# Kernel tuning notes

Hardware: AMD Instinct MI355X
Metric: run time of the kernel (lower is better)

## Reference

```python
import math
import jax, jax.numpy as jnp
import numpy as np

B, T, D = 2, 2048, 2048
DH, NQ, NKV = 128, 16, 4
QPG = NQ // NKV  # queries per group = 4
ROPE_BASE = 10000.0
YARN_SCALE = 2.0
ORIG_MAX_LEN = 4096
BETA_FAST, BETA_SLOW = 32.0, 1.0
EPS = 1.1920929e-07  # torch.finfo(float32).eps, RMSNorm default
MSCALE = 0.1 * math.log(YARN_SCALE) + 1.0
ATTN_SCALE = 1.0 / (MSCALE * math.sqrt(DH))


def _yarn_inv_freq():
    inv_freq = 1.0 / ROPE_BASE ** (np.arange(0, DH, 2, dtype=np.float32) / DH)
    wavelengths = 2.0 * math.pi / inv_freq
    low_w = ORIG_MAX_LEN / BETA_SLOW
    high_w = ORIG_MAX_LEN / BETA_FAST
    gamma = np.clip((low_w - wavelengths) / (low_w - high_w), 0.0, 1.0)
    return (gamma * inv_freq + (1.0 - gamma) * inv_freq / YARN_SCALE).astype(np.float32)


def setup_inputs() -> dict:
    key = jax.random.key(0)
    k0, k1, k2, k3 = jax.random.split(key, 4)
    x = jax.random.normal(k0, (B, T, D), jnp.float32)
    Wq = jax.random.normal(k1, (D, DH * NQ), jnp.float32) * 0.02
    Wkv = jax.random.normal(k2, (D, 2 * DH * NKV), jnp.float32) * 0.02
    Wout = jax.random.normal(k3, (DH * NQ, D), jnp.float32) * 0.02
    q_norm_w = jnp.ones((DH,), jnp.float32)
    k_norm_w = jnp.ones((DH,), jnp.float32)
    inv_freq = jnp.asarray(_yarn_inv_freq())
    return {"x": x, "Wq": Wq, "Wkv": Wkv, "Wout": Wout,
            "q_norm_w": q_norm_w, "k_norm_w": k_norm_w, "inv_freq": inv_freq}


def _rmsnorm(x, w):
    ms = jnp.mean(jnp.square(x), axis=-1, keepdims=True)
    return x * jax.lax.rsqrt(ms + EPS) * w


def _apply_rope(x, inv_freq):
    # x: (..., T, DH)
    t = jnp.arange(x.shape[-2], dtype=inv_freq.dtype)
    freqs = jnp.outer(t, inv_freq)               # (T, DH//2)
    emb = jnp.concatenate([freqs, freqs], -1)     # (T, DH)
    cos, sin = jnp.cos(emb), jnp.sin(emb)
    half = x.shape[-1] // 2
    x_rot = jnp.concatenate([-x[..., half:], x[..., :half]], -1)
    return x * cos + x_rot * sin


def reference(x, Wq, Wkv, Wout, q_norm_w, k_norm_w, inv_freq):
    q = x @ Wq                                    # (B, T, NQ*DH)
    kv = x @ Wkv                                  # (B, T, 2*NKV*DH)
    k, v = jnp.split(kv, 2, axis=-1)              # each (B, T, NKV*DH)
    # b t (qpg g d) -> b qpg g t d
    q = q.reshape(B, T, QPG, NKV, DH).transpose(0, 2, 3, 1, 4)
    # b t (g d) -> b g t d
    k = k.reshape(B, T, NKV, DH).transpose(0, 2, 1, 3)
    v = v.reshape(B, T, NKV, DH).transpose(0, 2, 1, 3)
    q = _apply_rope(_rmsnorm(q, q_norm_w), inv_freq)
    k = _apply_rope(_rmsnorm(k, k_norm_w), inv_freq)
    scores = jnp.einsum('bqgtd,bgsd->bqgts', q, k) * ATTN_SCALE
    causal = jnp.tril(jnp.ones((T, T), bool))
    scores = jnp.where(causal, scores, -jnp.inf)
    attn = jax.nn.softmax(scores, axis=-1)
    out = jnp.einsum('bqgts,bgsd->bqgtd', attn, v)
    # b qpg g t d -> b t (qpg g d)
    out = out.transpose(0, 3, 1, 2, 4).reshape(B, T, NQ * DH)
    return out @ Wout
```

## Files before the change

### kernel.cpp

```cpp
#include <hip/hip_runtime.h>
#include <math.h>


typedef __attribute__((ext_vector_type(8))) short s16x8;
typedef __attribute__((ext_vector_type(4))) float f32x4;
typedef __attribute__((ext_vector_type(4))) unsigned int u32x4;

__device__ __forceinline__ unsigned short f2bf(float x) {
  union { float f; unsigned int u; } v; v.f = x;
  return (unsigned short)((v.u + 0x7FFFu + ((v.u >> 16) & 1u)) >> 16);
}

__device__ __forceinline__ float bf2f(unsigned short x) {
  union { unsigned int u; float f; } v; v.u = (unsigned int)x << 16;
  return v.f;
}

__device__ __forceinline__ unsigned int cvt_pk_bf16(float lo, float hi) {
  unsigned int r;
  asm("v_cvt_pk_bf16_f32 %0, %1, %2" : "=v"(r) : "v"(lo), "v"(hi));
  return r;
}

#define GLD_LDS16(g, l)                                            \
  __builtin_amdgcn_global_load_lds(                                \
      (const __attribute__((address_space(1))) void*)(g),          \
      (__attribute__((address_space(3))) void*)(l), 16, 0, 0)

__device__ __forceinline__ void wtrans_body(const float* __restrict__ in,
                                            unsigned short* __restrict__ out,
                                            int R, int C, int bx, int by,
                                            unsigned short lt[64][65]) {
  const int r0 = bx * 64, c0 = by * 64;
  const int j = threadIdx.x & 63, i4 = threadIdx.x >> 6;
#pragma unroll
  for (int p = 0; p < 16; ++p) {
    int i = p * 4 + i4;
    lt[i][j] = f2bf(in[(size_t)(r0 + i) * C + c0 + j]);
  }
  __syncthreads();
#pragma unroll
  for (int p = 0; p < 16; ++p) {
    int i = p * 4 + i4;
    out[(size_t)(c0 + i) * R + r0 + j] = lt[j][i];
  }
}

__global__ __launch_bounds__(256) void prep1_k(const float* __restrict__ x,
                                               const float* __restrict__ Wq,
                                               const float* __restrict__ Wkv,
                                               const float* __restrict__ Wout,
                                               const float* __restrict__ invf,
                                               unsigned short* __restrict__ xb,
                                               unsigned short* __restrict__ wqkvt,
                                               unsigned short* __restrict__ wot,
                                               float2* __restrict__ cstab) {
  __shared__ unsigned short lt[64][65];
  const int bid = blockIdx.x;
  if (bid < 8192) {
    int i = bid * 256 + threadIdx.x;
    float4 v = ((const float4*)x)[i];
    unsigned long long pack = (unsigned long long)f2bf(v.x)
                            | ((unsigned long long)f2bf(v.y) << 16)
                            | ((unsigned long long)f2bf(v.z) << 32)
                            | ((unsigned long long)f2bf(v.w) << 48);
    ((unsigned long long*)xb)[i] = pack;
  } else if (bid < 9216) {
    int b2 = bid - 8192;
    wtrans_body(Wq, wqkvt, 2048, 2048, b2 & 31, b2 >> 5, lt);
  } else if (bid < 9728) {
    int b2 = bid - 9216;
    wtrans_body(Wkv, wqkvt + (size_t)2048 * 2048, 2048, 1024, b2 & 31, b2 >> 5, lt);
  } else if (bid < 10752) {
    int b2 = bid - 9728;
    wtrans_body(Wout, wot, 2048, 2048, b2 & 31, b2 >> 5, lt);
  } else {
    int i = (bid - 10752) * 256 + threadIdx.x;
    int t = i >> 6, f = i & 63;
    float s, c;
    sincosf((float)t * invf[f], &s, &c);
    cstab[i] = make_float2(c, s);
  }
}

template <int OUTBF>
__global__ __launch_bounds__(256) void gemm_bt_t(const unsigned short* __restrict__ A,
                                                 const unsigned short* __restrict__ Bt,
                                                 void* __restrict__ Cv,
                                                 int M, int N, int K) {
  __shared__ alignas(16) unsigned short sA[2][128][32];
  __shared__ alignas(16) unsigned short sB[2][128][32];
  const int tid = threadIdx.x;
  const int lane = tid & 63;
  const int w = tid >> 6;
  const int wm = (w >> 1) * 64, wn = (w & 1) * 64;
  const int nwg = gridDim.x * gridDim.y;
  int bid = blockIdx.y * gridDim.x + blockIdx.x;
  bid = (bid & 7) * (nwg >> 3) + (bid >> 3);
  const int m0 = (bid % gridDim.x) * 128, n0 = (bid / gridDim.x) * 128;
  const int l15 = lane & 15, lhi = lane >> 4;
  f32x4 acc[4][4];
#pragma unroll
  for (int i = 0; i < 4; ++i)
#pragma unroll
    for (int j = 0; j < 4; ++j) acc[i][j] = (f32x4){0.f, 0.f, 0.f, 0.f};
  const int row = tid >> 2;
  const int srcslot = (tid & 3) ^ ((row >> 1) & 3);
  const unsigned short* gA0 = A + (size_t)(m0 + row) * K + srcslot * 8;
  const unsigned short* gA1 = A + (size_t)(m0 + 64 + row) * K + srcslot * 8;
  const unsigned short* gB0 = Bt + (size_t)(n0 + row) * K + srcslot * 8;
  const unsigned short* gB1 = Bt + (size_t)(n0 + 64 + row) * K + srcslot * 8;
  char* ldsA = (char*)&sA[0][0][0] + w * 1024;
  char* ldsB = (char*)&sB[0][0][0] + w * 1024;
  auto STAGE = [&](int bb, int k0) {
    GLD_LDS16(gA0 + k0, ldsA + bb * 8192);
    GLD_LDS16(gA1 + k0, ldsA + bb * 8192 + 4096);
    GLD_LDS16(gB0 + k0, ldsB + bb * 8192);
    GLD_LDS16(gB1 + k0, ldsB + bb * 8192 + 4096);
  };
  const int sphys = (lhi ^ ((l15 >> 1) & 3)) * 8;
  const int nt = K >> 5;
  STAGE(0, 0);
  __syncthreads();
  int cur = 0;
  for (int t = 0; t < nt; ++t) {
    if (t + 1 < nt) STAGE(cur ^ 1, (t + 1) * 32);
    s16x8 af[4], bfr[4];
#pragma unroll
    for (int i = 0; i < 4; ++i) af[i] = *(const s16x8*)&sA[cur][wm + i * 16 + l15][sphys];
#pragma unroll
    for (int j = 0; j < 4; ++j) bfr[j] = *(const s16x8*)&sB[cur][wn + j * 16 + l15][sphys];
#pragma unroll
    for (int i = 0; i < 4; ++i)
#pragma unroll
      for (int j = 0; j < 4; ++j)
        acc[i][j] = __builtin_amdgcn_mfma_f32_16x16x32_bf16(af[i], bfr[j], acc[i][j], 0, 0, 0);
    __syncthreads();
    cur ^= 1;
  }
  const int col0 = n0 + wn + l15;
  const int row00 = m0 + wm + lhi * 4;
  if (OUTBF) {
    unsigned short* C = (unsigned short*)Cv;
#pragma unroll
    for (int i = 0; i < 4; ++i)
#pragma unroll
      for (int j = 0; j < 4; ++j)
#pragma unroll
        for (int r = 0; r < 4; ++r)
          C[(size_t)(row00 + i * 16 + r) * N + col0 + j * 16] = f2bf(acc[i][j][r]);
  } else {
    float* C = (float*)Cv;
#pragma unroll
    for (int i = 0; i < 4; ++i)
#pragma unroll
      for (int j = 0; j < 4; ++j)
#pragma unroll
        for (int r = 0; r < 4; ++r)
          C[(size_t)(row00 + i * 16 + r) * N + col0 + j * 16] = acc[i][j][r];
  }
}

__global__ __launch_bounds__(256) void prep2_k(const unsigned short* __restrict__ qkvb,
                                               const float* __restrict__ qw,
                                               const float* __restrict__ kw,
                                               const float2* __restrict__ cstab,
                                               unsigned short* __restrict__ qT,
                                               unsigned short* __restrict__ kT,
                                               unsigned short* __restrict__ vT) {
  __shared__ unsigned short lt[64][65];
  const int bid = blockIdx.x;
  if (bid < 20480) {
    constexpr float FOLD =
        (float)(1.4426950408889634 / ((0.1 * 0.6931471805599453 + 1.0) * 11.313708498984761));
    int wid = bid * 4 + (threadIdx.x >> 6);
    int lane = threadIdx.x & 63;
    const unsigned short* src; const float* wgt; unsigned short* dst;
    int t; float fold;
    if (wid < 65536) {
      int bt = wid >> 4, h = wid & 15;
      int b = bt >> 11; t = bt & 2047;
      src = qkvb + (size_t)bt * 3072 + h * 128;
      wgt = qw;
      dst = qT + ((size_t)(b * 16 + h) * 2048 + t) * 128;
      fold = FOLD;
    } else {
      int id = wid - 65536;
      int bt = id >> 2, g = id & 3;
      int b = bt >> 11; t = bt & 2047;
      src = qkvb + (size_t)bt * 3072 + 2048 + g * 128;
      wgt = kw;
      dst = kT + ((size_t)(b * 4 + g) * 2048 + t) * 128;
      fold = 1.0f;
    }
    unsigned int vv = ((const unsigned int*)src)[lane];
    float vx = bf2f((unsigned short)(vv & 0xffff));
    float vy = bf2f((unsigned short)(vv >> 16));
    float ss = vx * vx + vy * vy;
#pragma unroll
    for (int m = 32; m; m >>= 1) ss += __shfl_xor(ss, m);
    float rs = rsqrtf(ss * (1.0f / 128.0f) + 1.1920929e-07f);
    float2 wv = ((const float2*)wgt)[lane];
    float xn0 = vx * rs * wv.x;
    float xn1 = vy * rs * wv.y;
    float px = __shfl_xor(xn0, 32);
    float py = __shfl_xor(xn1, 32);
    float sgn = (lane < 32) ? -1.0f : 1.0f;
    int f0 = (2 * lane) & 63;
    float4 cs = ((const float4*)cstab)[((size_t)t * 64 + f0) >> 1];
    float r0 = (xn0 * cs.x + sgn * px * cs.y) * fold;
    float r1 = (xn1 * cs.z + sgn * py * cs.w) * fold;
    unsigned int packed = (unsigned int)f2bf(r0) | ((unsigned int)f2bf(r1) << 16);
    ((unsigned int*)dst)[lane] = packed;
  } else {
    int b2 = bid - 20480;
    const int tt0 = (b2 & 31) * 64;
    const int dd0 = ((b2 >> 5) & 1) * 64;
    const int z = b2 >> 6;
    const int b = z >> 2, g = z & 3;
    const int j = threadIdx.x & 63, i4 = threadIdx.x >> 6;
    const unsigned short* src = qkvb + (size_t)b * 2048 * 3072 + 2560 + g * 128 + dd0;
#pragma unroll
    for (int p = 0; p < 16; ++p) {
      int i = p * 4 + i4;
      lt[i][j] = src[(size_t)(tt0 + i) * 3072 + j];
    }
    __syncthreads();
    unsigned short* dst = vT + ((size_t)(b * 4 + g) * 128 + dd0) * 2048 + tt0;
    const int jp = (j & 32) | (((j & 15) >> 2) << 3) | (((j >> 4) & 1) << 2) | (j & 3);
#pragma unroll
    for (int p = 0; p < 16; ++p) {
      int d = p * 4 + i4;
      dst[(size_t)d * 2048 + jp] = lt[j][d];
    }
  }
}

__global__ __launch_bounds__(256) void attn_k(const unsigned short* __restrict__ qT,
                                              const unsigned short* __restrict__ kT,
                                              const unsigned short* __restrict__ vT,
                                              unsigned short* __restrict__ ao) {
  __shared__ alignas(16) unsigned short sK2[2][64][128];
  __shared__ alignas(16) unsigned short sV2[2][128][64];
  const int tid = threadIdx.x;
  const int lane = tid & 63;
  const int w = tid >> 6;
  const int l15 = lane & 15, lhi = lane >> 4;
  const int l8 = lane >> 3;
  const int bid = blockIdx.x;
  const int xg = bid & 7;
  const int b = xg >> 2, g = xg & 3;
  const int hh = (bid >> 3) & 3;
  const int h = hh * 4 + g;
  const int qt = 31 - (bid >> 5);
  const int q0 = qt * 64;
  const unsigned short* Qb = qT + ((size_t)(b * 16 + h) * 2048) * 128;
  const unsigned short* Kb = kT + ((size_t)(b * 4 + g) * 2048) * 128;
  const unsigned short* Vb = vT + ((size_t)(b * 4 + g) * 128) * 2048;

  s16x8 qfr[4];
#pragma unroll
  for (int ks = 0; ks < 4; ++ks)
    qfr[ks] = *(const s16x8*)(Qb + (size_t)(q0 + w * 16 + l15) * 128 + ks * 32 + lhi * 8);

  const int sgK = l15 ^ ((w * 4 + lhi) & 7);
  const int sgV = (lane & 7) ^ (l8 & 7);
  char* ldsK = (char*)&sK2[0][0][0] + w * 1024;
  char* ldsV = (char*)&sV2[0][0][0] + w * 1024;
  auto STAGEKV = [&](int bb, int kt) {
#pragma unroll
    for (int p = 0; p < 4; ++p) {
      GLD_LDS16(Kb + (size_t)(kt * 64 + p * 16 + w * 4 + lhi) * 128 + sgK * 8,
                ldsK + bb * 16384 + p * 4096);
      GLD_LDS16(Vb + (size_t)(p * 32 + w * 8 + l8) * 2048 + kt * 64 + sgV * 8,
                ldsV + bb * 16384 + p * 4096);
    }
  };
  const int xr = l15 & 7;

  f32x4 o[8];
#pragma unroll
  for (int i = 0; i < 8; ++i) o[i] = (f32x4){0.f, 0.f, 0.f, 0.f};
  f32x4 o9 = (f32x4){0.f, 0.f, 0.f, 0.f};
  s16x8 ones;
#pragma unroll
  for (int j = 0; j < 8; ++j) ones[j] = (short)0x3F80;

  STAGEKV(0, 0);
  int cur = 0;
  for (int kt = 0; kt <= qt; ++kt) {
    asm volatile("s_waitcnt vmcnt(0)" ::: "memory");
    __syncthreads();
    if (kt < qt) STAGEKV(cur ^ 1, kt + 1);
    f32x4 s[4];
#pragma unroll
    for (int jn = 0; jn < 4; ++jn) s[jn] = (f32x4){-16.f, -16.f, -16.f, -16.f};
#pragma unroll
    for (int ks = 0; ks < 4; ++ks)
#pragma unroll
      for (int jn = 0; jn < 4; ++jn) {
        s16x8 ak = *(const s16x8*)&sK2[cur][jn * 16 + l15][((ks * 4 + lhi) ^ xr) * 8];
        s[jn] = __builtin_amdgcn_mfma_f32_16x16x32_bf16(ak, qfr[ks], s[jn], 0, 0, 0);
      }
    if (kt == qt) {
#pragma unroll
      for (int jn = 0; jn < 4; ++jn)
#pragma unroll
        for (int r = 0; r < 4; ++r)
          if (jn * 16 + lhi * 4 + r > w * 16 + l15) s[jn][r] = -INFINITY;
    }
    float pp[4][4];
#pragma unroll
    for (int jn = 0; jn < 4; ++jn)
#pragma unroll
      for (int r = 0; r < 4; ++r) pp[jn][r] = exp2f(s[jn][r]);
    union { s16x8 v; unsigned int d[4]; } pa0, pa1;
#pragma unroll
    for (int d = 0; d < 2; ++d) {
      pa0.d[d]     = cvt_pk_bf16(pp[0][2 * d], pp[0][2 * d + 1]);
      pa0.d[2 + d] = cvt_pk_bf16(pp[1][2 * d], pp[1][2 * d + 1]);
      pa1.d[d]     = cvt_pk_bf16(pp[2][2 * d], pp[2][2 * d + 1]);
      pa1.d[2 + d] = cvt_pk_bf16(pp[3][2 * d], pp[3][2 * d + 1]);
    }
    o9 = __builtin_amdgcn_mfma_f32_16x16x32_bf16(pa0.v, ones, o9, 0, 0, 0);
    o9 = __builtin_amdgcn_mfma_f32_16x16x32_bf16(pa1.v, ones, o9, 0, 0, 0);
#pragma unroll
    for (int nt = 0; nt < 8; ++nt) {
      s16x8 vb0 = *(const s16x8*)&sV2[cur][nt * 16 + l15][(lhi ^ xr) * 8];
      o[nt] = __builtin_amdgcn_mfma_f32_16x16x32_bf16(pa0.v, vb0, o[nt], 0, 0, 0);
    }
#pragma unroll
    for (int nt = 0; nt < 8; ++nt) {
      s16x8 vb1 = *(const s16x8*)&sV2[cur][nt * 16 + l15][((lhi + 4) ^ xr) * 8];
      o[nt] = __builtin_amdgcn_mfma_f32_16x16x32_bf16(pa1.v, vb1, o[nt], 0, 0, 0);
    }
    cur ^= 1;
  }
#pragma unroll
  for (int r = 0; r < 4; ++r) {
    float invr = 1.0f / o9[r];
    int t = q0 + w * 16 + lhi * 4 + r;
    size_t base = ((size_t)b * 2048 + t) * 2048 + h * 128;
#pragma unroll
    for (int nt = 0; nt < 8; ++nt)
      ao[base + nt * 16 + l15] = f2bf(o[nt][r] * invr);
  }
}

extern "C" void kernel_launch(void* const* d_in, const int* in_sizes, int n_in,
                              void* d_out, int out_size, void* d_ws, size_t ws_size,
                              hipStream_t stream) {
  (void)in_sizes; (void)n_in; (void)out_size; (void)ws_size;
  const float* x    = (const float*)d_in[0];
  const float* Wq   = (const float*)d_in[1];
  const float* Wkv  = (const float*)d_in[2];
  const float* Wout = (const float*)d_in[3];
  const float* qw   = (const float*)d_in[4];
  const float* kw   = (const float*)d_in[5];
  const float* invf = (const float*)d_in[6];
  float* out = (float*)d_out;

  char* ws = (char*)d_ws;
  size_t off = 0;
  auto alloc = [&](size_t bytes) -> void* {
    void* p = ws + off; off += (bytes + 255) & ~(size_t)255; return p;
  };
  unsigned short* xb    = (unsigned short*)alloc((size_t)4096 * 2048 * 2);
  unsigned short* wqkvt = (unsigned short*)alloc((size_t)3072 * 2048 * 2);
  unsigned short* wot   = (unsigned short*)alloc((size_t)2048 * 2048 * 2);
  unsigned short* qkvb  = (unsigned short*)alloc((size_t)4096 * 3072 * 2);
  float2* cstab = (float2*)alloc((size_t)2048 * 64 * 8);
  unsigned short* qT = (unsigned short*)alloc((size_t)2 * 16 * 2048 * 128 * 2);
  unsigned short* kT = (unsigned short*)alloc((size_t)2 * 4 * 2048 * 128 * 2);
  unsigned short* vT = (unsigned short*)alloc((size_t)2 * 4 * 128 * 2048 * 2);
  unsigned short* ao = (unsigned short*)alloc((size_t)4096 * 2048 * 2);

  prep1_k<<<11264, 256, 0, stream>>>(x, Wq, Wkv, Wout, invf, xb, wqkvt, wot, cstab);
  gemm_bt_t<1><<<dim3(32, 24), 256, 0, stream>>>(xb, wqkvt, qkvb, 4096, 3072, 2048);
  prep2_k<<<20992, 256, 0, stream>>>(qkvb, qw, kw, cstab, qT, kT, vT);
  attn_k<<<1024, 256, 0, stream>>>(qT, kT, vT, ao);
  gemm_bt_t<0><<<dim3(32, 16), 256, 0, stream>>>(ao, wot, out, 4096, 2048, 2048);
}
```

Before: 193.6 us.

## Double attention query tile to 128 rows per block to reuse K/V tiles

```diff
diff --git a/kernel.cpp b/kernel.cpp
--- a/kernel.cpp
+++ b/kernel.cpp
@@ -252,16 +252,20 @@
   const int b = xg >> 2, g = xg & 3;
   const int hh = (bid >> 3) & 3;
   const int h = hh * 4 + g;
-  const int qt = 31 - (bid >> 5);
-  const int q0 = qt * 64;
+  const int u = bid >> 5;
+  const int qt = (u < 8) ? (15 - u) : (u - 8);
+  const int q0 = qt * 128;
   const unsigned short* Qb = qT + ((size_t)(b * 16 + h) * 2048) * 128;
   const unsigned short* Kb = kT + ((size_t)(b * 4 + g) * 2048) * 128;
   const unsigned short* Vb = vT + ((size_t)(b * 4 + g) * 128) * 2048;
 
-  s16x8 qfr[4];
-#pragma unroll
-  for (int ks = 0; ks < 4; ++ks)
-    qfr[ks] = *(const s16x8*)(Qb + (size_t)(q0 + w * 16 + l15) * 128 + ks * 32 + lhi * 8);
+  s16x8 qfr[2][4];
+#pragma unroll
+  for (int jq = 0; jq < 2; ++jq)
+#pragma unroll
+    for (int ks = 0; ks < 4; ++ks)
+      qfr[jq][ks] = *(const s16x8*)(Qb +
+          (size_t)(q0 + w * 32 + jq * 16 + l15) * 128 + ks * 32 + lhi * 8);
 
   const int sgK = l15 ^ ((w * 4 + lhi) & 7);
   const int sgV = (lane & 7) ^ (l8 & 7);
@@ -278,73 +282,89 @@
   };
   const int xr = l15 & 7;
 
-  f32x4 o[8];
-#pragma unroll
-  for (int i = 0; i < 8; ++i) o[i] = (f32x4){0.f, 0.f, 0.f, 0.f};
-  f32x4 o9 = (f32x4){0.f, 0.f, 0.f, 0.f};
+  f32x4 o[2][8];
+#pragma unroll
+  for (int jq = 0; jq < 2; ++jq)
+#pragma unroll
+    for (int i = 0; i < 8; ++i) o[jq][i] = (f32x4){0.f, 0.f, 0.f, 0.f};
+  f32x4 o9[2] = {(f32x4){0.f, 0.f, 0.f, 0.f}, (f32x4){0.f, 0.f, 0.f, 0.f}};
   s16x8 ones;
 #pragma unroll
   for (int j = 0; j < 8; ++j) ones[j] = (short)0x3F80;
 
+  const int ktmax = 2 * qt + 1;
   STAGEKV(0, 0);
   int cur = 0;
-  for (int kt = 0; kt <= qt; ++kt) {
+  for (int kt = 0; kt <= ktmax; ++kt) {
     asm volatile("s_waitcnt vmcnt(0)" ::: "memory");
     __syncthreads();
-    if (kt < qt) STAGEKV(cur ^ 1, kt + 1);
-    f32x4 s[4];
-#pragma unroll
-    for (int jn = 0; jn < 4; ++jn) s[jn] = (f32x4){-16.f, -16.f, -16.f, -16.f};
+    if (kt < ktmax) STAGEKV(cur ^ 1, kt + 1);
+    f32x4 s[2][4];
+#pragma unroll
+    for (int jq = 0; jq < 2; ++jq)
+#pragma unroll
+      for (int jn = 0; jn < 4; ++jn) s[jq][jn] = (f32x4){-16.f, -16.f, -16.f, -16.f};
 #pragma unroll
     for (int ks = 0; ks < 4; ++ks)
 #pragma unroll
       for (int jn = 0; jn < 4; ++jn) {
         s16x8 ak = *(const s16x8*)&sK2[cur][jn * 16 + l15][((ks * 4 + lhi) ^ xr) * 8];
-        s[jn] = __builtin_amdgcn_mfma_f32_16x16x32_bf16(ak, qfr[ks], s[jn], 0, 0, 0);
+        s[0][jn] = __builtin_amdgcn_mfma_f32_16x16x32_bf16(ak, qfr[0][ks], s[0][jn], 0, 0, 0);
+        s[1][jn] = __builtin_amdgcn_mfma_f32_16x16x32_bf16(ak, qfr[1][ks], s[1][jn], 0, 0, 0);
       }
-    if (kt == qt) {
+    if (kt >= 2 * qt) {
+#pragma unroll
+      for (int jq = 0; jq < 2; ++jq)
+#pragma unroll
+        for (int jn = 0; jn < 4; ++jn)
+#pragma unroll
+          for (int r = 0; r < 4; ++r)
+            if (kt * 64 + jn * 16 + lhi * 4 + r > q0 + w * 32 + jq * 16 + l15)
+              s[jq][jn][r] = -INFINITY;
+    }
+    union { s16x8 v; unsigned int d[4]; } pa[2][2];
+#pragma unroll
+    for (int jq = 0; jq < 2; ++jq) {
+      float pp[4][4];
 #pragma unroll
       for (int jn = 0; jn < 4; ++jn)
 #pragma unroll
-        for (int r = 0; r < 4; ++r)
-          if (jn * 16 + lhi * 4 + r > w * 16 + l15) s[jn][r] = -INFINITY;
-    }
-    float pp[4][4];
-#pragma unroll
-    for (int jn = 0; jn < 4; ++jn)
-#pragma unroll
-      for (int r = 0; r < 4; ++r) pp[jn][r] = exp2f(s[jn][r]);
-    union { s16x8 v; unsigned int d[4]; } pa0, pa1;
-#pragma unroll
-    for (int d = 0; d < 2; ++d) {
-      pa0.d[d]     = cvt_pk_bf16(pp[0][2 * d], pp[0][2 * d + 1]);
-      pa0.d[2 + d] = cvt_pk_bf16(pp[1][2 * d], pp[1][2 * d + 1]);
-      pa1.d[d]     = cvt_pk_bf16(pp[2][2 * d], pp[2][2 * d + 1]);
-      pa1.d[2 + d] = cvt_pk_bf16(pp[3][2 * d], pp[3][2 * d + 1]);
-    }
-    o9 = __builtin_amdgcn_mfma_f32_16x16x32_bf16(pa0.v, ones, o9, 0, 0, 0);
-    o9 = __builtin_amdgcn_mfma_f32_16x16x32_bf16(pa1.v, ones, o9, 0, 0, 0);
+        for (int r = 0; r < 4; ++r) pp[jn][r] = exp2f(s[jq][jn][r]);
+#pragma unroll
+      for (int d = 0; d < 2; ++d) {
+        pa[jq][0].d[d]     = cvt_pk_bf16(pp[0][2 * d], pp[0][2 * d + 1]);
+        pa[jq][0].d[2 + d] = cvt_pk_bf16(pp[1][2 * d], pp[1][2 * d + 1]);
+        pa[jq][1].d[d]     = cvt_pk_bf16(pp[2][2 * d], pp[2][2 * d + 1]);
+        pa[jq][1].d[2 + d] = cvt_pk_bf16(pp[3][2 * d], pp[3][2 * d + 1]);
+      }
+      o9[jq] = __builtin_amdgcn_mfma_f32_16x16x32_bf16(pa[jq][0].v, ones, o9[jq], 0, 0, 0);
+      o9[jq] = __builtin_amdgcn_mfma_f32_16x16x32_bf16(pa[jq][1].v, ones, o9[jq], 0, 0, 0);
+    }
 #pragma unroll
     for (int nt = 0; nt < 8; ++nt) {
       s16x8 vb0 = *(const s16x8*)&sV2[cur][nt * 16 + l15][(lhi ^ xr) * 8];
-      o[nt] = __builtin_amdgcn_mfma_f32_16x16x32_bf16(pa0.v, vb0, o[nt], 0, 0, 0);
+      o[0][nt] = __builtin_amdgcn_mfma_f32_16x16x32_bf16(pa[0][0].v, vb0, o[0][nt], 0, 0, 0);
+      o[1][nt] = __builtin_amdgcn_mfma_f32_16x16x32_bf16(pa[1][0].v, vb0, o[1][nt], 0, 0, 0);
     }
 #pragma unroll
     for (int nt = 0; nt < 8; ++nt) {
       s16x8 vb1 = *(const s16x8*)&sV2[cur][nt * 16 + l15][((lhi + 4) ^ xr) * 8];
-      o[nt] = __builtin_amdgcn_mfma_f32_16x16x32_bf16(pa1.v, vb1, o[nt], 0, 0, 0);
+      o[0][nt] = __builtin_amdgcn_mfma_f32_16x16x32_bf16(pa[0][1].v, vb1, o[0][nt], 0, 0, 0);
+      o[1][nt] = __builtin_amdgcn_mfma_f32_16x16x32_bf16(pa[1][1].v, vb1, o[1][nt], 0, 0, 0);
     }
     cur ^= 1;
   }
 #pragma unroll
-  for (int r = 0; r < 4; ++r) {
-    float invr = 1.0f / o9[r];
-    int t = q0 + w * 16 + lhi * 4 + r;
-    size_t base = ((size_t)b * 2048 + t) * 2048 + h * 128;
-#pragma unroll
-    for (int nt = 0; nt < 8; ++nt)
-      ao[base + nt * 16 + l15] = f2bf(o[nt][r] * invr);
-  }
+  for (int jq = 0; jq < 2; ++jq)
+#pragma unroll
+    for (int r = 0; r < 4; ++r) {
+      float invr = 1.0f / o9[jq][r];
+      int t = q0 + w * 32 + jq * 16 + lhi * 4 + r;
+      size_t base = ((size_t)b * 2048 + t) * 2048 + h * 128;
+#pragma unroll
+      for (int nt = 0; nt < 8; ++nt)
+        ao[base + nt * 16 + l15] = f2bf(o[jq][nt][r] * invr);
+    }
 }
 
 extern "C" void kernel_launch(void* const* d_in, const int* in_sizes, int n_in,
@@ -378,6 +398,6 @@
   prep1_k<<<11264, 256, 0, stream>>>(x, Wq, Wkv, Wout, invf, xb, wqkvt, wot, cstab);
   gemm_bt_t<1><<<dim3(32, 24), 256, 0, stream>>>(xb, wqkvt, qkvb, 4096, 3072, 2048);
   prep2_k<<<20992, 256, 0, stream>>>(qkvb, qw, kw, cstab, qT, kT, vT);
-  attn_k<<<1024, 256, 0, stream>>>(qT, kT, vT, ao);
+  attn_k<<<512, 256, 0, stream>>>(qT, kT, vT, ao);
   gemm_bt_t<0><<<dim3(32, 16), 256, 0, stream>>>(ao, wot, out, 4096, 2048, 2048);
 }
```

Result: slower. 207.0 us (+6.9%).
